# Optimization experiments

Measured on AMD Instinct MI355X. Metric: run time of the kernel, lower is better.

Reference implementation:

```python
import jax, jax.numpy as jnp
import numpy as np

HEADS = 16
EMBED = 1024
HEAD_DIM = EMBED // HEADS


def setup_inputs() -> dict:
    key = jax.random.key(0)
    ks = jax.random.split(key, 10)
    B, SQ, SKV = 2, 2048, 2048
    s = 1.0 / np.sqrt(HEAD_DIM)
    sd = 1.0 / np.sqrt(EMBED)
    return {
        "queries": jax.random.normal(ks[0], (B, SQ, EMBED), jnp.float32),
        "values": jax.random.normal(ks[1], (B, SKV, EMBED), jnp.float32),
        "heads": HEADS,
        "Wv": jax.random.normal(ks[2], (HEAD_DIM, HEAD_DIM), jnp.float32) * s,
        "bv": jax.random.normal(ks[3], (HEAD_DIM,), jnp.float32) * 0.02,
        "Wk": jax.random.normal(ks[4], (HEAD_DIM, HEAD_DIM), jnp.float32) * s,
        "bk": jax.random.normal(ks[5], (HEAD_DIM,), jnp.float32) * 0.02,
        "Wq": jax.random.normal(ks[6], (HEAD_DIM, HEAD_DIM), jnp.float32) * s,
        "bq": jax.random.normal(ks[7], (HEAD_DIM,), jnp.float32) * 0.02,
        "Wd": jax.random.normal(ks[8], (EMBED, EMBED), jnp.float32) * sd,
        "bd": jax.random.normal(ks[9], (EMBED,), jnp.float32) * 0.02,
    }


def reference(queries, values, heads, Wv, bv, Wk, bk, Wq, bq, Wd, bd):
    n, sq, e = queries.shape
    skv = values.shape[1]
    d = e // heads
    # reshape to per-head layout [b, s, h, d]
    q_in = queries.reshape(n, sq, heads, d)
    v_in = values.reshape(n, skv, heads, d)
    # shared per-head linear projections (torch Linear: x @ W.T + b)
    v = jnp.einsum("bshd,ed->bshe", v_in, Wv) + bv
    # quirk preserved: keys computed from the ALREADY-PROJECTED values
    k = jnp.einsum("bshd,ed->bshe", v, Wk) + bk
    q = jnp.einsum("bshd,ed->bshe", q_in, Wq) + bq
    # full O(n^2) score matrix [b, h, sq, skv] (as in source)
    scores = jnp.einsum("bqhd,bkhd->bhqk", q, k) / jnp.sqrt(jnp.asarray(d, q.dtype))
    attn = jax.nn.softmax(scores, axis=-1)
    out = jnp.einsum("bhqk,bkhd->bqhd", attn, v).reshape(n, sq, e)
    return out @ Wd.T + bd
```

## Files before the change

### kernel.cpp

```cpp
#include <hip/hip_runtime.h>
#include <hip/hip_bf16.h>
#include <hip/hip_fp16.h>
#include <math.h>

typedef _Float16 f16;
typedef _Float16 f16x8 __attribute__((ext_vector_type(8)));
typedef _Float16 f16x4 __attribute__((ext_vector_type(4)));
typedef _Float16 f16x2 __attribute__((ext_vector_type(2)));
typedef unsigned short u16x8v __attribute__((ext_vector_type(8)));
typedef float f32x4 __attribute__((ext_vector_type(4)));

namespace {
constexpr int B = 2;
constexpr int H = 16;
constexpr int S = 2048;
constexpr int D = 64;
constexpr int E = 1024;
constexpr float QSCALE = 0.125f * 1.4426950408889634f;
}

#define GLOBAL_LOAD_LDS16(gp, lp)                                              \
  __builtin_amdgcn_global_load_lds(                                            \
      (const __attribute__((address_space(1))) void*)(gp),                     \
      (__attribute__((address_space(3))) void*)(lp), 16, 0, 0)

__global__ __launch_bounds__(256) void prep(const float* __restrict__ Wd, f16* __restrict__ wd16,
                                            const float* __restrict__ Wk, const float* __restrict__ Wv,
                                            const float* __restrict__ bv, const float* __restrict__ bk,
                                            float* __restrict__ Wkv, float* __restrict__ bkv) {
  if (blockIdx.x < 1024) {
    const int i = blockIdx.x * 256 + threadIdx.x;
    const float4 f = ((const float4*)Wd)[i];
    f16x4 o;
    o.x = (f16)f.x; o.y = (f16)f.y; o.z = (f16)f.z; o.w = (f16)f.w;
    *(f16x4*)(wd16 + 4 * (size_t)i) = o;
  } else {
    const int g = (blockIdx.x - 1024) * 256 + threadIdx.x;
    const int i = g >> 6, j = g & 63;
    float s = 0.f;
#pragma unroll 16
    for (int d = 0; d < 64; ++d) s = fmaf(Wk[i * 64 + d], Wv[d * 64 + j], s);
    Wkv[g] = s;
    if (g < 64) {
      float bb = bk[g];
#pragma unroll 16
      for (int d = 0; d < 64; ++d) bb = fmaf(Wk[g * 64 + d], bv[d], bb);
      bkv[g] = bb;
    }
  }
}

__global__ __launch_bounds__(256) void proj3_mfma(const float* __restrict__ xq,
                                                  const float* __restrict__ xv,
                                                  const float* __restrict__ Wq,
                                                  const float* __restrict__ bq,
                                                  const float* __restrict__ Wv,
                                                  const float* __restrict__ bv,
                                                  const float* __restrict__ Wkv,
                                                  const float* __restrict__ bkv,
                                                  f16* __restrict__ qp,
                                                  f16* __restrict__ vp,
                                                  f16* __restrict__ kp) {
  const int which = blockIdx.y;
  const float* x = which ? xv : xq;

  const int t = threadIdx.x, lane = t & 63, w = t >> 6;
  const int l15 = lane & 15, quad = lane >> 4;
  const int m0 = (blockIdx.x * 4 + w) * 64;

  f16x8 af[4][2];
#pragma unroll
  for (int mt = 0; mt < 4; ++mt)
#pragma unroll
    for (int kc = 0; kc < 2; ++kc) {
      const float* g = x + (size_t)(m0 + mt * 16 + l15) * 64 + kc * 32 + quad * 8;
      const float4 a = *(const float4*)g, b2 = *(const float4*)(g + 4);
      f16x8 v;
      v[0]=(f16)a.x; v[1]=(f16)a.y; v[2]=(f16)a.z; v[3]=(f16)a.w;
      v[4]=(f16)b2.x; v[5]=(f16)b2.y; v[6]=(f16)b2.z; v[7]=(f16)b2.w;
      af[mt][kc] = v;
    }

  const int npass = which ? 2 : 1;
  for (int pass = 0; pass < npass; ++pass) {
    const float* W    = which ? (pass ? Wkv : Wv) : Wq;
    const float* bias = which ? (pass ? bkv : bv) : bq;
    f16* out          = which ? (pass ? kp : vp) : qp;
    const float scale = which ? 1.0f : QSCALE;

    f16x8 wf[4][2];
#pragma unroll
    for (int nt = 0; nt < 4; ++nt)
#pragma unroll
      for (int kc = 0; kc < 2; ++kc) {
        const float* g = W + (size_t)(nt * 16 + l15) * 64 + kc * 32 + quad * 8;
        const float4 a = *(const float4*)g, b2 = *(const float4*)(g + 4);
        f16x8 v;
        v[0]=(f16)a.x; v[1]=(f16)a.y; v[2]=(f16)a.z; v[3]=(f16)a.w;
        v[4]=(f16)b2.x; v[5]=(f16)b2.y; v[6]=(f16)b2.z; v[7]=(f16)b2.w;
        wf[nt][kc] = v;
      }

    f32x4 acc[4][4];
#pragma unroll
    for (int nt = 0; nt < 4; ++nt)
#pragma unroll
      for (int mt = 0; mt < 4; ++mt) acc[nt][mt] = (f32x4){0.f, 0.f, 0.f, 0.f};
#pragma unroll
    for (int kc = 0; kc < 2; ++kc)
#pragma unroll
      for (int nt = 0; nt < 4; ++nt)
#pragma unroll
        for (int mt = 0; mt < 4; ++mt)
          acc[nt][mt] = __builtin_amdgcn_mfma_f32_16x16x32_f16(wf[nt][kc], af[mt][kc], acc[nt][mt], 0, 0, 0);

    float4 bl4[4];
#pragma unroll
    for (int nt = 0; nt < 4; ++nt) bl4[nt] = *(const float4*)&bias[nt * 16 + quad * 4];

#pragma unroll
    for (int mt = 0; mt < 4; ++mt) {
      const int g = m0 + mt * 16 + l15;
      const int h = g & 15, bs_ = g >> 4;
      const int b = bs_ >> 11, s = bs_ & 2047;
      f16* o = out + ((size_t)(b * H + h) * S + s) * 64 + quad * 4;
#pragma unroll
      for (int nt = 0; nt < 4; ++nt) {
        const float p0 = (acc[nt][mt][0] + bl4[nt].x) * scale;
        const float p1 = (acc[nt][mt][1] + bl4[nt].y) * scale;
        const float p2 = (acc[nt][mt][2] + bl4[nt].z) * scale;
        const float p3 = (acc[nt][mt][3] + bl4[nt].w) * scale;
        union { f16x4 v4; f16x2 hh[2]; } u;
        u.hh[0] = __builtin_bit_cast(f16x2, __builtin_amdgcn_cvt_pkrtz(p0, p1));
        u.hh[1] = __builtin_bit_cast(f16x2, __builtin_amdgcn_cvt_pkrtz(p2, p3));
        *(f16x4*)(o + nt * 16) = u.v4;
      }
    }
  }
}

__global__ __launch_bounds__(256) void attn_mfma(const f16* __restrict__ qp,
                                                 const f16* __restrict__ kp,
                                                 const f16* __restrict__ vp,
                                                 f16* __restrict__ ao) {
  __shared__ f16 vt[2][64 * 64];
  const int t = threadIdx.x, lane = t & 63, w = t >> 6;
  const int l15 = lane & 15, quad = lane >> 4;
  const int bh = blockIdx.x;
  const int q0 = blockIdx.y * 128;
  const f16* qbase = qp + ((size_t)bh * S + q0 + w * 32) * D;
  const f16* kbase = kp + (size_t)bh * S * D;
  const f16* vbase = vp + (size_t)bh * S * D;

  const int vd0 = (t >> 5) * 8;
  const int p0 = (t & 31) * 2;
  const int vkv = ((p0 >> 5) << 5) | (((p0 & 7) >> 2) << 4) | (((p0 >> 3) & 3) << 2) | (p0 & 3);
  const int vchunk = p0 >> 3, vsub = p0 & 7;

  const f16* kfbase = kbase + (size_t)l15 * D + quad * 8;

  f16x8 qf[2][2];
#pragma unroll
  for (int mt = 0; mt < 2; ++mt)
#pragma unroll
    for (int kc = 0; kc < 2; ++kc)
      qf[mt][kc] = *(const f16x8*)(qbase + (size_t)(mt * 16 + l15) * D + kc * 32 + quad * 8);

  f16x8 vb4;
#pragma unroll
  for (int j = 0; j < 8; ++j) vb4[j] = (l15 == 0) ? (f16)1.0f : (f16)0.0f;

  f32x4 O[2][5];
#pragma unroll
  for (int mt = 0; mt < 2; ++mt)
#pragma unroll
    for (int nt = 0; nt < 5; ++nt) O[mt][nt] = (f32x4){0.f, 0.f, 0.f, 0.f};

  f16x8 kf[2][4][2];
#pragma unroll
  for (int nt = 0; nt < 4; ++nt)
#pragma unroll
    for (int kc = 0; kc < 2; ++kc)
      kf[0][nt][kc] = *(const f16x8*)(kfbase + (size_t)(nt * 16) * D + kc * 32);

  u16x8v va, vb2;
  {
    const f16* gv = vbase + (size_t)vkv * D + vd0;
    va  = *(const u16x8v*)gv;
    vb2 = *(const u16x8v*)(gv + D);
#pragma unroll
    for (int j = 0; j < 8; ++j) {
      const int d = vd0 + j;
      const unsigned pk = (unsigned)va[j] | ((unsigned)vb2[j] << 16);
      *(unsigned*)&vt[0][d * 64 + ((vchunk ^ (d & 7)) * 8) + vsub] = pk;
    }
  }

  for (int kt2 = 0; kt2 < S / 64; kt2 += 2) {
#pragma unroll
    for (int half = 0; half < 2; ++half) {
      const int kt = kt2 + half;
      if (kt + 1 < S / 64) {
        const f16* kn = kfbase + (size_t)((kt + 1) * 64) * D;
#pragma unroll
        for (int nt = 0; nt < 4; ++nt)
#pragma unroll
          for (int kc = 0; kc < 2; ++kc)
            kf[half ^ 1][nt][kc] = *(const f16x8*)(kn + (size_t)(nt * 16) * D + kc * 32);
        const f16* gv = vbase + ((size_t)(kt + 1) * 64 + vkv) * D + vd0;
        va  = *(const u16x8v*)gv;
        vb2 = *(const u16x8v*)(gv + D);
      }
      __asm__ volatile("s_waitcnt lgkmcnt(0)" ::: "memory");
      __builtin_amdgcn_s_barrier();
      __asm__ volatile("" ::: "memory");

      f32x4 sc[4][2];
#pragma unroll
      for (int nt = 0; nt < 4; ++nt)
#pragma unroll
        for (int mt = 0; mt < 2; ++mt) sc[nt][mt] = (f32x4){0.f, 0.f, 0.f, 0.f};
      __builtin_amdgcn_s_setprio(1);
#pragma unroll
      for (int kc = 0; kc < 2; ++kc)
#pragma unroll
        for (int nt = 0; nt < 4; ++nt)
#pragma unroll
          for (int mt = 0; mt < 2; ++mt)
            sc[nt][mt] = __builtin_amdgcn_mfma_f32_16x16x32_f16(kf[half][nt][kc], qf[mt][kc], sc[nt][mt], 0, 0, 0);
      __builtin_amdgcn_s_setprio(0);

      f16x8 pa[2][2];
#pragma unroll
      for (int mt = 0; mt < 2; ++mt)
#pragma unroll
        for (int kc = 0; kc < 2; ++kc) {
          const f32x4 s0 = sc[2 * kc][mt], s1 = sc[2 * kc + 1][mt];
          union { f16x8 v8; f16x2 h[4]; } u;
          u.h[0] = __builtin_bit_cast(f16x2, __builtin_amdgcn_cvt_pkrtz(
              __builtin_amdgcn_exp2f(s0[0]), __builtin_amdgcn_exp2f(s0[1])));
          u.h[1] = __builtin_bit_cast(f16x2, __builtin_amdgcn_cvt_pkrtz(
              __builtin_amdgcn_exp2f(s0[2]), __builtin_amdgcn_exp2f(s0[3])));
          u.h[2] = __builtin_bit_cast(f16x2, __builtin_amdgcn_cvt_pkrtz(
              __builtin_amdgcn_exp2f(s1[0]), __builtin_amdgcn_exp2f(s1[1])));
          u.h[3] = __builtin_bit_cast(f16x2, __builtin_amdgcn_cvt_pkrtz(
              __builtin_amdgcn_exp2f(s1[2]), __builtin_amdgcn_exp2f(s1[3])));
          pa[mt][kc] = u.v8;
        }

      __builtin_amdgcn_s_setprio(1);
#pragma unroll
      for (int kc = 0; kc < 2; ++kc) {
#pragma unroll
        for (int nt = 0; nt < 4; ++nt) {
          const f16x8 vbf = *(const f16x8*)&vt[half][(nt * 16 + l15) * 64 + (((kc * 4 + quad) ^ (l15 & 7)) * 8)];
#pragma unroll
          for (int mt = 0; mt < 2; ++mt)
            O[mt][nt] = __builtin_amdgcn_mfma_f32_16x16x32_f16(pa[mt][kc], vbf, O[mt][nt], 0, 0, 0);
        }
#pragma unroll
        for (int mt = 0; mt < 2; ++mt)
          O[mt][4] = __builtin_amdgcn_mfma_f32_16x16x32_f16(pa[mt][kc], vb4, O[mt][4], 0, 0, 0);
      }
      __builtin_amdgcn_s_setprio(0);

      if (kt + 1 < S / 64) {
#pragma unroll
        for (int j = 0; j < 8; ++j) {
          const int d = vd0 + j;
          const unsigned pk = (unsigned)va[j] | ((unsigned)vb2[j] << 16);
          *(unsigned*)&vt[half ^ 1][d * 64 + ((vchunk ^ (d & 7)) * 8) + vsub] = pk;
        }
      }
    }
  }

  const int b = bh >> 4, h = bh & 15;
#pragma unroll
  for (int mt = 0; mt < 2; ++mt)
#pragma unroll
    for (int r = 0; r < 4; ++r) {
      const float l = __shfl(O[mt][4][r], quad << 4, 64);
      const float inv = 1.f / l;
      const int row = q0 + w * 32 + mt * 16 + quad * 4 + r;
      f16* o = ao + ((size_t)b * S + row) * E + h * D;
#pragma unroll
      for (int nt = 0; nt < 4; ++nt)
        o[nt * 16 + l15] = (f16)(O[mt][nt][r] * inv);
    }
}

__global__ __launch_bounds__(256) void dense_mfma(const f16* __restrict__ A,
                                                  const f16* __restrict__ Wd16,
                                                  const float* __restrict__ bd,
                                                  float* __restrict__ out) {
  __shared__ f16 as[2][128 * 64];
  __shared__ f16 bs[2][64 * 64];
  const int t = threadIdx.x;
  const int lane = t & 63;
  const int w = t >> 6;
  const int l15 = lane & 15;
  const int quad = lane >> 4;
  const int m0 = blockIdx.x * 128;
  const int n0 = blockIdx.y * 64;
  const int wm = (w >> 1) * 64, wn = (w & 1) * 32;

  const int srow = (lane >> 3);
  const int schunk = (lane & 7) ^ srow;
  const f16* ga0 = A    + (size_t)(m0 + w * 32 + srow) * E + schunk * 8;
  const f16* gb0 = Wd16 + (size_t)(n0 + w * 16 + srow) * E + schunk * 8;

  constexpr int NT = E / 64;

  f32x4 acc[4][2];
#pragma unroll
  for (int mt = 0; mt < 4; ++mt)
#pragma unroll
    for (int nt = 0; nt < 2; ++nt) acc[mt][nt] = (f32x4){0.f, 0.f, 0.f, 0.f};

#pragma unroll
  for (int i = 0; i < 4; ++i)
    GLOBAL_LOAD_LDS16(ga0 + (size_t)(i * 8) * E, &as[0][(w * 32 + i * 8) * 64]);
#pragma unroll
  for (int i = 0; i < 2; ++i)
    GLOBAL_LOAD_LDS16(gb0 + (size_t)(i * 8) * E, &bs[0][(w * 16 + i * 8) * 64]);
  __syncthreads();

  int cur = 0;
  for (int kt = 0; kt < NT; ++kt) {
    if (kt + 1 < NT) {
      const int nb = cur ^ 1;
#pragma unroll
      for (int i = 0; i < 4; ++i)
        GLOBAL_LOAD_LDS16(ga0 + (size_t)(i * 8) * E + (kt + 1) * 64, &as[nb][(w * 32 + i * 8) * 64]);
#pragma unroll
      for (int i = 0; i < 2; ++i)
        GLOBAL_LOAD_LDS16(gb0 + (size_t)(i * 8) * E + (kt + 1) * 64, &bs[nb][(w * 16 + i * 8) * 64]);
    }
    f16x8 af[4][2];
#pragma unroll
    for (int mt = 0; mt < 4; ++mt)
#pragma unroll
      for (int kc = 0; kc < 2; ++kc)
        af[mt][kc] = *(const f16x8*)&as[cur][(wm + mt * 16 + l15) * 64 + (((kc * 4 + quad) ^ (l15 & 7)) * 8)];
#pragma unroll
    for (int kc = 0; kc < 2; ++kc)
#pragma unroll
      for (int nt = 0; nt < 2; ++nt) {
        const f16x8 bf = *(const f16x8*)&bs[cur][(wn + nt * 16 + l15) * 64 + (((kc * 4 + quad) ^ (l15 & 7)) * 8)];
#pragma unroll
        for (int mt = 0; mt < 4; ++mt)
          acc[mt][nt] = __builtin_amdgcn_mfma_f32_16x16x32_f16(af[mt][kc], bf, acc[mt][nt], 0, 0, 0);
      }
    __syncthreads();
    cur ^= 1;
  }

#pragma unroll
  for (int nt = 0; nt < 2; ++nt) {
    const int col = n0 + wn + nt * 16 + l15;
    const float bdv = bd[col];
#pragma unroll
    for (int mt = 0; mt < 4; ++mt)
#pragma unroll
      for (int r = 0; r < 4; ++r)
        out[(size_t)(m0 + wm + mt * 16 + quad * 4 + r) * E + col] = acc[mt][nt][r] + bdv;
  }
}

extern "C" void kernel_launch(void* const* d_in, const int* in_sizes, int n_in,
                              void* d_out, int out_size, void* d_ws, size_t ws_size,
                              hipStream_t stream) {
  const float* queries = (const float*)d_in[0];
  const float* values  = (const float*)d_in[1];
  const float* Wv = (const float*)d_in[3];
  const float* bv = (const float*)d_in[4];
  const float* Wk = (const float*)d_in[5];
  const float* bk = (const float*)d_in[6];
  const float* Wq = (const float*)d_in[7];
  const float* bq = (const float*)d_in[8];
  const float* Wd = (const float*)d_in[9];
  const float* bd = (const float*)d_in[10];
  float* out = (float*)d_out;

  char* ws = (char*)d_ws;
  f16* qp    = (f16*)(ws);
  f16* kp    = (f16*)(ws + 8u * 1024 * 1024);
  f16* vp    = (f16*)(ws + 16u * 1024 * 1024);
  f16* ao    = (f16*)(ws + 24u * 1024 * 1024);
  f16* wd16  = (f16*)(ws + 32u * 1024 * 1024);
  float* wkv = (float*)(ws + 34u * 1024 * 1024);
  float* bkv = (float*)(ws + 34u * 1024 * 1024 + 16384);
  (void)ws_size; (void)in_sizes; (void)n_in; (void)out_size;

  prep<<<1040, 256, 0, stream>>>(Wd, wd16, Wk, Wv, bv, bk, wkv, bkv);
  proj3_mfma<<<dim3(256, 2), 256, 0, stream>>>(queries, values, Wq, bq, Wv, bv, wkv, bkv, qp, vp, kp);
  attn_mfma<<<dim3(B * H, S / 128), 256, 0, stream>>>(qp, kp, vp, ao);
  dense_mfma<<<dim3(B * S / 128, E / 64), 256, 0, stream>>>(ao, wd16, bd, out);
}
```

Before: 206.7 us.

## Write V pre-transposed in projection and triple-buffer K/V via direct global-to-LDS loads

The projection kernel now stages the V output in shared memory and writes it transposed ([b,h,d,s] with a permuted key order), so the attention kernel no longer transposes V through registers into LDS. The attention kernel drops register-prefetched K and the manual V transpose. Instead it issues async global_load_lds for both K and V tiles into a 3-deep LDS ring with XOR swizzle, waiting on vmcnt before each tile. This is meant to hide global latency and cut VGPR pressure, at the cost of more LDS (48KB) and extra shared-memory traffic and barriers in the projection kernel.

```diff
diff --git a/kernel.cpp b/kernel.cpp
--- a/kernel.cpp
+++ b/kernel.cpp
@@ -59,8 +59,9 @@
                                                   const float* __restrict__ Wkv,
                                                   const float* __restrict__ bkv,
                                                   f16* __restrict__ qp,
-                                                  f16* __restrict__ vp,
+                                                  f16* __restrict__ vtp,
                                                   f16* __restrict__ kp) {
+  __shared__ f16 tb[16 * 16 * 64];
   const int which = blockIdx.y;
   const float* x = which ? xv : xq;
 
@@ -85,7 +86,8 @@
   for (int pass = 0; pass < npass; ++pass) {
     const float* W    = which ? (pass ? Wkv : Wv) : Wq;
     const float* bias = which ? (pass ? bkv : bv) : bq;
-    f16* out          = which ? (pass ? kp : vp) : qp;
+    const bool vpass  = (which == 1) && (pass == 0);
+    f16* out          = which ? (pass ? kp : (f16*)nullptr) : qp;
     const float scale = which ? 1.0f : QSCALE;
 
     f16x8 wf[4][2];
@@ -123,7 +125,7 @@
       const int g = m0 + mt * 16 + l15;
       const int h = g & 15, bs_ = g >> 4;
       const int b = bs_ >> 11, s = bs_ & 2047;
-      f16* o = out + ((size_t)(b * H + h) * S + s) * 64 + quad * 4;
+      f16* o = vpass ? nullptr : (out + ((size_t)(b * H + h) * S + s) * 64 + quad * 4);
 #pragma unroll
       for (int nt = 0; nt < 4; ++nt) {
         const float p0 = (acc[nt][mt][0] + bl4[nt].x) * scale;
@@ -133,31 +135,65 @@
         union { f16x4 v4; f16x2 hh[2]; } u;
         u.hh[0] = __builtin_bit_cast(f16x2, __builtin_amdgcn_cvt_pkrtz(p0, p1));
         u.hh[1] = __builtin_bit_cast(f16x2, __builtin_amdgcn_cvt_pkrtz(p2, p3));
-        *(f16x4*)(o + nt * 16) = u.v4;
-      }
+        if (vpass) {
+#pragma unroll
+          for (int r = 0; r < 4; ++r)
+            tb[(l15 * 64 + nt * 16 + quad * 4 + r) * 16 + w * 4 + mt] = u.v4[r];
+        } else {
+          *(f16x4*)(o + nt * 16) = u.v4;
+        }
+      }
+    }
+
+    if (vpass) {
+      __syncthreads();
+      const int bsb = blockIdx.x * 16;
+      const int bb = bsb >> 11;
+      const int sb = bsb & 2047;
+      const int off = sb & 63;
+      const int poff = (off & 32) | ((off & 16) >> 2);
+      const int col0 = (sb - off) + poff;
+#pragma unroll
+      for (int k2 = 0; k2 < 4; ++k2) {
+        const int pi = t * 4 + k2;
+        const int h = pi >> 6, d = pi & 63;
+        const f16x8 lo = *(const f16x8*)&tb[pi * 16];
+        const f16x8 hi = *(const f16x8*)&tb[pi * 16 + 8];
+        f16* orow = vtp + ((size_t)(bb * H + h) * 64 + d) * S + col0;
+        f16x4 g0, g1, g2, g3;
+#pragma unroll
+        for (int j = 0; j < 4; ++j) { g0[j]=lo[j]; g1[j]=lo[4+j]; g2[j]=hi[j]; g3[j]=hi[4+j]; }
+        *(f16x4*)(orow + 0)  = g0;
+        *(f16x4*)(orow + 8)  = g1;
+        *(f16x4*)(orow + 16) = g2;
+        *(f16x4*)(orow + 24) = g3;
+      }
+      __syncthreads();
     }
   }
 }
 
 __global__ __launch_bounds__(256) void attn_mfma(const f16* __restrict__ qp,
                                                  const f16* __restrict__ kp,
-                                                 const f16* __restrict__ vp,
+                                                 const f16* __restrict__ vtp,
                                                  f16* __restrict__ ao) {
-  __shared__ f16 vt[2][64 * 64];
+  __shared__ f16 ks[3][64 * 64];
+  __shared__ f16 vs[3][64 * 64];
   const int t = threadIdx.x, lane = t & 63, w = t >> 6;
   const int l15 = lane & 15, quad = lane >> 4;
   const int bh = blockIdx.x;
   const int q0 = blockIdx.y * 128;
   const f16* qbase = qp + ((size_t)bh * S + q0 + w * 32) * D;
   const f16* kbase = kp + (size_t)bh * S * D;
-  const f16* vbase = vp + (size_t)bh * S * D;
-
-  const int vd0 = (t >> 5) * 8;
-  const int p0 = (t & 31) * 2;
-  const int vkv = ((p0 >> 5) << 5) | (((p0 & 7) >> 2) << 4) | (((p0 >> 3) & 3) << 2) | (p0 & 3);
-  const int vchunk = p0 >> 3, vsub = p0 & 7;
-
-  const f16* kfbase = kbase + (size_t)l15 * D + quad * 8;
+  const f16* vtbase = vtp + (size_t)bh * 64 * S;
+
+  const int c1 = w * 64 + lane;
+  const int row1 = c1 >> 3;
+  const int sc1 = (c1 & 7) ^ (row1 & 7);
+  const size_t koff1 = (size_t)row1 * D + sc1 * 8;
+  const size_t koff2 = koff1 + (size_t)32 * D;
+  const size_t voff1 = (size_t)row1 * S + sc1 * 8;
+  const size_t voff2 = voff1 + (size_t)32 * S;
 
   f16x8 qf[2][2];
 #pragma unroll
@@ -176,104 +212,85 @@
 #pragma unroll
     for (int nt = 0; nt < 5; ++nt) O[mt][nt] = (f32x4){0.f, 0.f, 0.f, 0.f};
 
-  f16x8 kf[2][4][2];
-#pragma unroll
-  for (int nt = 0; nt < 4; ++nt)
+#define ISSUE_TILE(tt, buf)                                                    \
+  {                                                                            \
+    const f16* gk = kbase + (size_t)(tt) * (64 * D);                           \
+    GLOBAL_LOAD_LDS16(gk + koff1, &ks[buf][w * 512]);                          \
+    GLOBAL_LOAD_LDS16(gk + koff2, &ks[buf][2048 + w * 512]);                   \
+    const f16* gv = vtbase + (size_t)(tt) * 64;                                \
+    GLOBAL_LOAD_LDS16(gv + voff1, &vs[buf][w * 512]);                          \
+    GLOBAL_LOAD_LDS16(gv + voff2, &vs[buf][2048 + w * 512]);                   \
+  }
+
+  ISSUE_TILE(0, 0);
+  ISSUE_TILE(1, 1);
+
+  int rb = 0;
+  for (int kt = 0; kt < S / 64; ++kt) {
+    __asm__ volatile("s_waitcnt vmcnt(4)" ::: "memory");
+    __builtin_amdgcn_s_barrier();
+    __builtin_amdgcn_sched_barrier(0);
+
+    {
+      const int tt = (kt + 2 < S / 64) ? (kt + 2) : (S / 64 - 1);
+      const int ib = (rb + 2 >= 3) ? (rb - 1) : (rb + 2);
+      ISSUE_TILE(tt, ib);
+    }
+
+    f32x4 sc[4][2];
+#pragma unroll
+    for (int nt = 0; nt < 4; ++nt)
+#pragma unroll
+      for (int mt = 0; mt < 2; ++mt) sc[nt][mt] = (f32x4){0.f, 0.f, 0.f, 0.f};
+    __builtin_amdgcn_s_setprio(1);
 #pragma unroll
     for (int kc = 0; kc < 2; ++kc)
-      kf[0][nt][kc] = *(const f16x8*)(kfbase + (size_t)(nt * 16) * D + kc * 32);
-
-  u16x8v va, vb2;
-  {
-    const f16* gv = vbase + (size_t)vkv * D + vd0;
-    va  = *(const u16x8v*)gv;
-    vb2 = *(const u16x8v*)(gv + D);
-#pragma unroll
-    for (int j = 0; j < 8; ++j) {
-      const int d = vd0 + j;
-      const unsigned pk = (unsigned)va[j] | ((unsigned)vb2[j] << 16);
-      *(unsigned*)&vt[0][d * 64 + ((vchunk ^ (d & 7)) * 8) + vsub] = pk;
-    }
-  }
-
-  for (int kt2 = 0; kt2 < S / 64; kt2 += 2) {
-#pragma unroll
-    for (int half = 0; half < 2; ++half) {
-      const int kt = kt2 + half;
-      if (kt + 1 < S / 64) {
-        const f16* kn = kfbase + (size_t)((kt + 1) * 64) * D;
-#pragma unroll
-        for (int nt = 0; nt < 4; ++nt)
-#pragma unroll
-          for (int kc = 0; kc < 2; ++kc)
-            kf[half ^ 1][nt][kc] = *(const f16x8*)(kn + (size_t)(nt * 16) * D + kc * 32);
-        const f16* gv = vbase + ((size_t)(kt + 1) * 64 + vkv) * D + vd0;
-        va  = *(const u16x8v*)gv;
-        vb2 = *(const u16x8v*)(gv + D);
-      }
-      __asm__ volatile("s_waitcnt lgkmcnt(0)" ::: "memory");
-      __builtin_amdgcn_s_barrier();
-      __asm__ volatile("" ::: "memory");
-
-      f32x4 sc[4][2];
-#pragma unroll
-      for (int nt = 0; nt < 4; ++nt)
-#pragma unroll
-        for (int mt = 0; mt < 2; ++mt) sc[nt][mt] = (f32x4){0.f, 0.f, 0.f, 0.f};
-      __builtin_amdgcn_s_setprio(1);
-#pragma unroll
-      for (int kc = 0; kc < 2; ++kc)
-#pragma unroll
-        for (int nt = 0; nt < 4; ++nt)
-#pragma unroll
-          for (int mt = 0; mt < 2; ++mt)
-            sc[nt][mt] = __builtin_amdgcn_mfma_f32_16x16x32_f16(kf[half][nt][kc], qf[mt][kc], sc[nt][mt], 0, 0, 0);
-      __builtin_amdgcn_s_setprio(0);
-
-      f16x8 pa[2][2];
+#pragma unroll
+      for (int nt = 0; nt < 4; ++nt) {
+        const f16x8 kf = *(const f16x8*)&ks[rb][(nt * 16 + l15) * 64 + (((kc * 4 + quad) ^ (l15 & 7)) * 8)];
+#pragma unroll
+        for (int mt = 0; mt < 2; ++mt)
+          sc[nt][mt] = __builtin_amdgcn_mfma_f32_16x16x32_f16(kf, qf[mt][kc], sc[nt][mt], 0, 0, 0);
+      }
+    __builtin_amdgcn_s_setprio(0);
+
+    f16x8 pa[2][2];
+#pragma unroll
+    for (int mt = 0; mt < 2; ++mt)
+#pragma unroll
+      for (int kc = 0; kc < 2; ++kc) {
+        const f32x4 s0 = sc[2 * kc][mt], s1 = sc[2 * kc + 1][mt];
+        union { f16x8 v8; f16x2 h[4]; } u;
+        u.h[0] = __builtin_bit_cast(f16x2, __builtin_amdgcn_cvt_pkrtz(
+            __builtin_amdgcn_exp2f(s0[0]), __builtin_amdgcn_exp2f(s0[1])));
+        u.h[1] = __builtin_bit_cast(f16x2, __builtin_amdgcn_cvt_pkrtz(
+            __builtin_amdgcn_exp2f(s0[2]), __builtin_amdgcn_exp2f(s0[3])));
+        u.h[2] = __builtin_bit_cast(f16x2, __builtin_amdgcn_cvt_pkrtz(
+            __builtin_amdgcn_exp2f(s1[0]), __builtin_amdgcn_exp2f(s1[1])));
+        u.h[3] = __builtin_bit_cast(f16x2, __builtin_amdgcn_cvt_pkrtz(
+            __builtin_amdgcn_exp2f(s1[2]), __builtin_amdgcn_exp2f(s1[3])));
+        pa[mt][kc] = u.v8;
+      }
+
+    __builtin_amdgcn_s_setprio(1);
+#pragma unroll
+    for (int kc = 0; kc < 2; ++kc) {
+#pragma unroll
+      for (int nt = 0; nt < 4; ++nt) {
+        const f16x8 vbf = *(const f16x8*)&vs[rb][(nt * 16 + l15) * 64 + (((kc * 4 + quad) ^ (l15 & 7)) * 8)];
+#pragma unroll
+        for (int mt = 0; mt < 2; ++mt)
+          O[mt][nt] = __builtin_amdgcn_mfma_f32_16x16x32_f16(pa[mt][kc], vbf, O[mt][nt], 0, 0, 0);
+      }
 #pragma unroll
       for (int mt = 0; mt < 2; ++mt)
-#pragma unroll
-        for (int kc = 0; kc < 2; ++kc) {
-          const f32x4 s0 = sc[2 * kc][mt], s1 = sc[2 * kc + 1][mt];
-          union { f16x8 v8; f16x2 h[4]; } u;
-          u.h[0] = __builtin_bit_cast(f16x2, __builtin_amdgcn_cvt_pkrtz(
-              __builtin_amdgcn_exp2f(s0[0]), __builtin_amdgcn_exp2f(s0[1])));
-          u.h[1] = __builtin_bit_cast(f16x2, __builtin_amdgcn_cvt_pkrtz(
-              __builtin_amdgcn_exp2f(s0[2]), __builtin_amdgcn_exp2f(s0[3])));
-          u.h[2] = __builtin_bit_cast(f16x2, __builtin_amdgcn_cvt_pkrtz(
-              __builtin_amdgcn_exp2f(s1[0]), __builtin_amdgcn_exp2f(s1[1])));
-          u.h[3] = __builtin_bit_cast(f16x2, __builtin_amdgcn_cvt_pkrtz(
-              __builtin_amdgcn_exp2f(s1[2]), __builtin_amdgcn_exp2f(s1[3])));
-          pa[mt][kc] = u.v8;
-        }
-
-      __builtin_amdgcn_s_setprio(1);
-#pragma unroll
-      for (int kc = 0; kc < 2; ++kc) {
-#pragma unroll
-        for (int nt = 0; nt < 4; ++nt) {
-          const f16x8 vbf = *(const f16x8*)&vt[half][(nt * 16 + l15) * 64 + (((kc * 4 + quad) ^ (l15 & 7)) * 8)];
-#pragma unroll
-          for (int mt = 0; mt < 2; ++mt)
-            O[mt][nt] = __builtin_amdgcn_mfma_f32_16x16x32_f16(pa[mt][kc], vbf, O[mt][nt], 0, 0, 0);
-        }
-#pragma unroll
-        for (int mt = 0; mt < 2; ++mt)
-          O[mt][4] = __builtin_amdgcn_mfma_f32_16x16x32_f16(pa[mt][kc], vb4, O[mt][4], 0, 0, 0);
-      }
-      __builtin_amdgcn_s_setprio(0);
-
-      if (kt + 1 < S / 64) {
-#pragma unroll
-        for (int j = 0; j < 8; ++j) {
-          const int d = vd0 + j;
-          const unsigned pk = (unsigned)va[j] | ((unsigned)vb2[j] << 16);
-          *(unsigned*)&vt[half ^ 1][d * 64 + ((vchunk ^ (d & 7)) * 8) + vsub] = pk;
-        }
-      }
-    }
-  }
+        O[mt][4] = __builtin_amdgcn_mfma_f32_16x16x32_f16(pa[mt][kc], vb4, O[mt][4], 0, 0, 0);
+    }
+    __builtin_amdgcn_s_setprio(0);
+
+    rb = (rb + 1 >= 3) ? 0 : rb + 1;
+  }
+#undef ISSUE_TILE
 
   const int b = bh >> 4, h = bh & 15;
 #pragma unroll
@@ -386,7 +403,7 @@
   char* ws = (char*)d_ws;
   f16* qp    = (f16*)(ws);
   f16* kp    = (f16*)(ws + 8u * 1024 * 1024);
-  f16* vp    = (f16*)(ws + 16u * 1024 * 1024);
+  f16* vtp   = (f16*)(ws + 16u * 1024 * 1024);
   f16* ao    = (f16*)(ws + 24u * 1024 * 1024);
   f16* wd16  = (f16*)(ws + 32u * 1024 * 1024);
   float* wkv = (float*)(ws + 34u * 1024 * 1024);
@@ -394,7 +411,7 @@
   (void)ws_size; (void)in_sizes; (void)n_in; (void)out_size;
 
   prep<<<1040, 256, 0, stream>>>(Wd, wd16, Wk, Wv, bv, bk, wkv, bkv);
-  proj3_mfma<<<dim3(256, 2), 256, 0, stream>>>(queries, values, Wq, bq, Wv, bv, wkv, bkv, qp, vp, kp);
-  attn_mfma<<<dim3(B * H, S / 128), 256, 0, stream>>>(qp, kp, vp, ao);
+  proj3_mfma<<<dim3(256, 2), 256, 0, stream>>>(queries, values, Wq, bq, Wv, bv, wkv, bkv, qp, vtp, kp);
+  attn_mfma<<<dim3(B * H, S / 128), 256, 0, stream>>>(qp, kp, vtp, ao);
   dense_mfma<<<dim3(B * S / 128, E / 64), 256, 0, stream>>>(ao, wd16, bd, out);
 }
```

Measured after the change: 184.0 us. -11.0%, faster.
